# Performance work log

Hardware: AMD Instinct MI355X
Metric: run time of the kernel (lower is better)

The kernel has to match this reference:

```python
import jax, jax.numpy as jnp
import numpy as np

N = 50000      # num nodes
E = 800000     # num edges
IN = 512       # in_feats (= num_hidden)
H = 8          # num_heads
D = 64         # out_feats per head (H*D = 512)
NEG_SLOPE = 0.2


def setup_inputs() -> dict:
    key = jax.random.key(0)
    ks = jax.random.split(key, 7)
    feat = jax.random.normal(ks[0], (N, IN), jnp.float32)
    src = jax.random.randint(ks[1], (E,), 0, N)
    dst = jax.random.randint(ks[2], (E,), 0, N)
    W_fc = jax.random.normal(ks[3], (IN, H * D), jnp.float32) * (1.0 / np.sqrt(IN))
    W_res = jax.random.normal(ks[4], (IN, H * D), jnp.float32) * (1.0 / np.sqrt(IN))
    attn_l = jax.random.normal(ks[5], (1, H, D), jnp.float32) * 0.1
    attn_r = jax.random.normal(ks[6], (1, H, D), jnp.float32) * 0.1
    return {"feat": feat, "src": src, "dst": dst, "W_fc": W_fc,
            "W_res": W_res, "attn_l": attn_l, "attn_r": attn_r}


def reference(feat, src, dst, W_fc, W_res, attn_l, attn_r):
    # fc: [N, IN] @ [IN, H*D] -> [N, H, D]
    ft = (feat @ W_fc).reshape(N, H, D)
    # attention logits per node: el = sum(ft * attn_l, -1), er likewise -> [N, H]
    el = jnp.sum(ft * attn_l, axis=-1)
    er = jnp.sum(ft * attn_r, axis=-1)
    # u_add_v on edges, then LeakyReLU -> [E, H]
    e = jax.nn.leaky_relu(el[src] + er[dst], negative_slope=NEG_SLOPE)
    # edge_softmax: normalize over incoming edges of each dst node
    m = jax.ops.segment_max(e, dst, num_segments=N)            # [N, H]
    m = jnp.where(jnp.isfinite(m), m, jnp.zeros_like(m))       # guard zero-in-degree
    ex = jnp.exp(e - m[dst])                                   # [E, H]
    s = jax.ops.segment_sum(ex, dst, num_segments=N)           # [N, H]
    a = ex / jnp.maximum(s[dst], 1e-9)                         # [E, H]
    # u_mul_e + sum aggregation: gather src features, weight, scatter-add to dst
    msg = ft[src] * a[:, :, None]                              # [E, H, D]
    rst = jax.ops.segment_sum(msg, dst, num_segments=N)        # [N, H, D]
    # residual: res_fc Linear since in_dst_feats != out_feats
    rst = rst + (feat @ W_res).reshape(N, H, D)
    return rst
```

## Files before the change

kernel.cpp:

```cpp
#include <hip/hip_runtime.h>
#include <hip/hip_bf16.h>

#define NN 50000
#define EE 800000
#define INF 512
#define HH 8
#define DD 64
#define HD 512

typedef unsigned short u16;
typedef u16 u16x8 __attribute__((ext_vector_type(8)));
typedef __bf16 bf16x8 __attribute__((ext_vector_type(8)));
typedef float f32x4 __attribute__((ext_vector_type(4)));

__device__ __forceinline__ float bf2f(u16 u) {
    return __uint_as_float(((unsigned)u) << 16);
}
__device__ __forceinline__ u16 f2bf(float f) {
    __hip_bfloat16 h = __float2bfloat16(f);
    return *reinterpret_cast<u16*>(&h);
}

__device__ __forceinline__ void gload_lds16(const void* g, void* l) {
    __builtin_amdgcn_global_load_lds(
        (const __attribute__((address_space(1))) void*)g,
        (__attribute__((address_space(3))) void*)l, 16, 0, 0);
}

__global__ __launch_bounds__(256) void sniff5_kernel(const u16* __restrict__ p0,
                                                     const u16* __restrict__ p1,
                                                     const u16* __restrict__ p2,
                                                     const u16* __restrict__ p3,
                                                     const u16* __restrict__ p4,
                                                     int* __restrict__ flags) {
    const u16* ps[5] = {p0, p1, p2, p3, p4};
    const u16* p = ps[blockIdx.x];
    __shared__ int bad;
    if (threadIdx.x == 0) bad = 0;
    __syncthreads();
    float v = fabsf(bf2f(p[2 * threadIdx.x]));
    if (!(v < 1e4f)) atomicAdd(&bad, 1);
    __syncthreads();
    if (threadIdx.x == 0) flags[blockIdx.x] = (bad >= 8) ? 1 : 0;
}

__global__ __launch_bounds__(256) void convert_kernel(const void* __restrict__ in,
                                                      u16* __restrict__ out,
                                                      const int* __restrict__ flag) {
    const int isf32 = *flag;
    const int total = NN * INF / 8;
    for (int i = blockIdx.x * 256 + threadIdx.x; i < total; i += gridDim.x * 256) {
        if (isf32) {
            f32x4 a = ((const f32x4*)in)[2 * i];
            f32x4 b = ((const f32x4*)in)[2 * i + 1];
            u16x8 w;
#pragma unroll
            for (int j = 0; j < 4; ++j) { w[j] = f2bf(a[j]); w[4 + j] = f2bf(b[j]); }
            ((u16x8*)out)[i] = w;
        } else {
            ((u16x8*)out)[i] = ((const u16x8*)in)[i];
        }
    }
}

__global__ __launch_bounds__(256) void transpose_kernel(const void* __restrict__ in,
                                                        u16* __restrict__ out,
                                                        const int* __restrict__ flag) {
    __shared__ u16 tile[64][65];
    const int isf32 = *flag;
    int tr = (blockIdx.x & 7) * 64;
    int tc = (blockIdx.x >> 3) * 64;
    for (int idx = threadIdx.x; idx < 64 * 64; idx += 256) {
        int r = idx >> 6, c = idx & 63;
        int g = (tr + r) * 512 + tc + c;
        tile[r][c] = isf32 ? f2bf(((const float*)in)[g]) : ((const u16*)in)[g];
    }
    __syncthreads();
    for (int idx = threadIdx.x; idx < 64 * 64; idx += 256) {
        int r = idx >> 6, c = idx & 63;
        out[(tc + r) * 512 + tr + c] = tile[c][r];
    }
}

__global__ void zero_deg_kernel(int* __restrict__ deg) {
    int t = blockIdx.x * 256 + threadIdx.x;
    if (t < NN) deg[t] = 0;
}

__global__ void count_kernel(const int* __restrict__ dst, int* __restrict__ deg) {
    int e = blockIdx.x * 256 + threadIdx.x;
    if (e < EE) atomicAdd(&deg[dst[e]], 1);
}

#define SCAN_CH 49
__global__ __launch_bounds__(1024) void scan_kernel(const int* __restrict__ deg,
                                                    int* __restrict__ rowptr,
                                                    int* __restrict__ cursor) {
    __shared__ int sums[1024];
    int t = threadIdx.x;
    int base = t * SCAN_CH;
    int s = 0;
    for (int k = 0; k < SCAN_CH; ++k) {
        int i = base + k;
        if (i < NN) s += deg[i];
    }
    sums[t] = s;
    __syncthreads();
    for (int off = 1; off < 1024; off <<= 1) {
        int v = (t >= off) ? sums[t - off] : 0;
        __syncthreads();
        sums[t] += v;
        __syncthreads();
    }
    int run = (t == 0) ? 0 : sums[t - 1];
    for (int k = 0; k < SCAN_CH; ++k) {
        int i = base + k;
        if (i < NN) {
            rowptr[i] = run;
            cursor[i] = run;
            run += deg[i];
        }
    }
    if (t == 0) rowptr[NN] = EE;
}

__global__ void scatter_kernel(const int* __restrict__ src, const int* __restrict__ dst,
                               int* __restrict__ cursor, int* __restrict__ csr_src) {
    int e = blockIdx.x * 256 + threadIdx.x;
    if (e < EE) {
        int p = atomicAdd(&cursor[dst[e]], 1);
        csr_src[p] = src[e];
    }
}

#define TM 128
#define TN 128
#define BK 64
#define NT (INF / BK)
#define NMBLK 392

__global__ __launch_bounds__(256, 5) void gemm_kernel(const u16* __restrict__ Ab,
                                                      const u16* __restrict__ Wt,
                                                      u16* __restrict__ ft,
                                                      float* __restrict__ outf) {
    __shared__ u16 Asm[TM * BK];
    __shared__ u16 Bsm[TN * BK];

    const int bid = blockIdx.x;
    const int r8 = bid & 7;
    const int q = bid >> 3;
    const int m0 = (((q >> 3) << 3) | r8) * TM;
    const int n0 = (q & 7) * TN;
    const int tid = threadIdx.x;
    const int lane = tid & 63;
    const int wave = tid >> 6;
    const int wr = (wave >> 1) * 64;
    const int wc = (wave & 1) * 64;
    const int lrow = lane & 15;
    const int quad = lane >> 4;

    const int rg = lane >> 3;
    const int ch = lane & 7;
    const int cs = ch ^ rg;

    const u16* asrc[4];
    const u16* bsrc[4];
    u16* adst[4];
    u16* bdst[4];
#pragma unroll
    for (int g = 0; g < 4; ++g) {
        int G = wave * 4 + g;
        int r = G * 8 + rg;
        int gr = m0 + r; gr = gr < NN ? gr : NN - 1;
        asrc[g] = Ab + (size_t)gr * INF + cs * 8;
        bsrc[g] = Wt + (size_t)(n0 + r) * INF + cs * 8;
        adst[g] = Asm + G * 512;
        bdst[g] = Bsm + G * 512;
    }

    f32x4 acc[4][4] = {};

    for (int t = 0; t < NT; ++t) {
        const int k0 = t * BK;
        __syncthreads();
#pragma unroll
        for (int g = 0; g < 4; ++g) {
            gload_lds16(asrc[g] + k0, adst[g]);
            gload_lds16(bsrc[g] + k0, bdst[g]);
        }
        __syncthreads();

#pragma unroll
        for (int ks = 0; ks < 2; ++ks) {
            bf16x8 af[4], bfr[4];
#pragma unroll
            for (int mi = 0; mi < 4; ++mi) {
                int ar = wr + mi * 16 + lrow;
                int sc = (ks * 4 + quad) ^ (ar & 7);
                u16x8 tv = *(const u16x8*)(Asm + ar * 64 + sc * 8);
                af[mi] = *(bf16x8*)&tv;
            }
#pragma unroll
            for (int ni = 0; ni < 4; ++ni) {
                int br = wc + ni * 16 + lrow;
                int sc = (ks * 4 + quad) ^ (br & 7);
                u16x8 tv = *(const u16x8*)(Bsm + br * 64 + sc * 8);
                bfr[ni] = *(bf16x8*)&tv;
            }
#pragma unroll
            for (int mi = 0; mi < 4; ++mi)
#pragma unroll
                for (int ni = 0; ni < 4; ++ni)
                    acc[mi][ni] = __builtin_amdgcn_mfma_f32_16x16x32_bf16(af[mi], bfr[ni],
                                                                          acc[mi][ni], 0, 0, 0);
        }
    }

#pragma unroll
    for (int mi = 0; mi < 4; ++mi) {
        int rb = m0 + wr + mi * 16 + quad * 4;
#pragma unroll
        for (int ni = 0; ni < 4; ++ni) {
            int col = n0 + wc + ni * 16 + lrow;
#pragma unroll
            for (int r = 0; r < 4; ++r) {
                int row = rb + r;
                if (row < NN) {
                    float v = acc[mi][ni][r];
                    if (col < HD) ft[row * HD + col] = f2bf(v);
                    else outf[row * HD + (col - HD)] = v;
                }
            }
        }
    }
}

__global__ __launch_bounds__(256) void attn_dot_kernel(const u16* __restrict__ ft,
                                                       const void* __restrict__ al,
                                                       const void* __restrict__ ar,
                                                       float* __restrict__ el,
                                                       float* __restrict__ er,
                                                       const int* __restrict__ flags) {
    int node = blockIdx.x * 4 + (threadIdx.x >> 6);
    if (node >= NN) return;
    int lane = threadIdx.x & 63;
    int off = lane * 8;

    float wl[8], wr_[8];
    if (flags[3]) {
        f32x4 a0 = *(const f32x4*)((const float*)al + off);
        f32x4 a1 = *(const f32x4*)((const float*)al + off + 4);
#pragma unroll
        for (int j = 0; j < 4; ++j) { wl[j] = a0[j]; wl[4 + j] = a1[j]; }
    } else {
        u16x8 a = *(const u16x8*)((const u16*)al + off);
#pragma unroll
        for (int j = 0; j < 8; ++j) wl[j] = bf2f(a[j]);
    }
    if (flags[4]) {
        f32x4 a0 = *(const f32x4*)((const float*)ar + off);
        f32x4 a1 = *(const f32x4*)((const float*)ar + off + 4);
#pragma unroll
        for (int j = 0; j < 4; ++j) { wr_[j] = a0[j]; wr_[4 + j] = a1[j]; }
    } else {
        u16x8 a = *(const u16x8*)((const u16*)ar + off);
#pragma unroll
        for (int j = 0; j < 8; ++j) wr_[j] = bf2f(a[j]);
    }

    u16x8 f = *(const u16x8*)(ft + node * HD + off);
    float vl = 0.0f, vr = 0.0f;
#pragma unroll
    for (int j = 0; j < 8; ++j) {
        float x = bf2f(f[j]);
        vl += x * wl[j];
        vr += x * wr_[j];
    }
#pragma unroll
    for (int msk = 1; msk < 8; msk <<= 1) {
        vl += __shfl_xor(vl, msk);
        vr += __shfl_xor(vr, msk);
    }
    if ((lane & 7) == 0) {
        el[node * HH + (lane >> 3)] = vl;
        er[node * HH + (lane >> 3)] = vr;
    }
}

__global__ __launch_bounds__(256) void aggregate_kernel(const int* __restrict__ rowptr,
                                                        const int* __restrict__ csr_src,
                                                        const u16* __restrict__ ft,
                                                        const float* __restrict__ el,
                                                        const float* __restrict__ er,
                                                        float* __restrict__ outf) {
    int node = blockIdx.x * 4 + (threadIdx.x >> 6);
    if (node >= NN) return;
    int lane = threadIdx.x & 63;
    int head = lane >> 3;
    int beg = rowptr[node], end = rowptr[node + 1];
    float erd = er[node * HH + head];

    float m = -INFINITY;
    float sden = 0.0f;
    float acc[8] = {};

    float el_n = 0.0f;
    u16x8 f_n = {};
    if (beg < end) {
        int s0 = csr_src[beg];
        el_n = el[s0 * HH + head];
        f_n = *(const u16x8*)(ft + s0 * HD + lane * 8);
    }
    for (int i = beg; i < end; ++i) {
        float elv = el_n;
        u16x8 f = f_n;
        if (i + 1 < end) {
            int s2 = csr_src[i + 1];
            el_n = el[s2 * HH + head];
            f_n = *(const u16x8*)(ft + s2 * HD + lane * 8);
        }
        float v = elv + erd;
        v = v > 0.0f ? v : 0.2f * v;
        float nm = fmaxf(m, v);
        float scale = __expf(m - nm);
        float ex = __expf(v - nm);
        m = nm;
        sden = sden * scale + ex;
#pragma unroll
        for (int j = 0; j < 8; ++j) acc[j] = acc[j] * scale + bf2f(f[j]) * ex;
    }

    float inv = 1.0f / fmaxf(sden, 1e-9f);
    float* op = outf + node * HD + lane * 8;
    f32x4 r0 = *(const f32x4*)op;
    f32x4 r1 = *(const f32x4*)(op + 4);
    f32x4 o0, o1;
#pragma unroll
    for (int j = 0; j < 4; ++j) {
        o0[j] = acc[j] * inv + r0[j];
        o1[j] = acc[4 + j] * inv + r1[j];
    }
    *(f32x4*)op = o0;
    *(f32x4*)(op + 4) = o1;
}

extern "C" void kernel_launch(void* const* d_in, const int* in_sizes, int n_in,
                              void* d_out, int out_size, void* d_ws, size_t ws_size,
                              hipStream_t stream) {
    const void* feat   = d_in[0];
    const int*  src    = (const int*)d_in[1];
    const int*  dst    = (const int*)d_in[2];
    const void* W_fc   = d_in[3];
    const void* W_res  = d_in[4];
    const void* attn_l = d_in[5];
    const void* attn_r = d_in[6];
    float* outf = (float*)d_out;

    char* ws = (char*)d_ws;
    int*   flags   = (int*)(ws);
    u16*   Wt      = (u16*)(ws + 256);
    u16*   ft      = (u16*)(ws + 1048832);
    float* el      = (float*)(ws + 52248832);
    float* er      = (float*)(ws + 53848832);
    int*   deg     = (int*)(ws + 55448832);
    int*   rowptr  = (int*)(ws + 55648832);
    int*   cursor  = (int*)(ws + 55848896);
    int*   csr_src = (int*)(ws + 56048896);
    u16*   feat16  = (u16*)(ws + 59248896);

    sniff5_kernel<<<5, 256, 0, stream>>>((const u16*)feat, (const u16*)W_fc,
                                         (const u16*)W_res, (const u16*)attn_l,
                                         (const u16*)attn_r, flags);
    convert_kernel<<<2048, 256, 0, stream>>>(feat, feat16, flags + 0);
    transpose_kernel<<<64, 256, 0, stream>>>(W_fc, Wt, flags + 1);
    transpose_kernel<<<64, 256, 0, stream>>>(W_res, Wt + 512 * 512, flags + 2);

    zero_deg_kernel<<<(NN + 255) / 256, 256, 0, stream>>>(deg);
    count_kernel<<<(EE + 255) / 256, 256, 0, stream>>>(dst, deg);
    scan_kernel<<<1, 1024, 0, stream>>>(deg, rowptr, cursor);
    scatter_kernel<<<(EE + 255) / 256, 256, 0, stream>>>(src, dst, cursor, csr_src);

    gemm_kernel<<<NMBLK * 8, 256, 0, stream>>>(feat16, Wt, ft, outf);

    attn_dot_kernel<<<(NN + 3) / 4, 256, 0, stream>>>(ft, attn_l, attn_r, el, er, flags);
    aggregate_kernel<<<(NN + 3) / 4, 256, 0, stream>>>(rowptr, csr_src, ft, el, er, outf);
}
```

Before: 679.0 us.

## Split aggregation across two waves per node with 4-deep gather prefetch and no online max

The aggregate kernel now assigns two wavefronts per destination node, each lane handling 4 features instead of 8, and unrolls the edge loop by four with a software pipeline that keeps four gathers in flight plus source indices prefetched two steps ahead. The online-softmax running max and rescaling are dropped in favour of a plain exp with the logit clamped at 75, so the per-edge work needs fewer exps and multiplies. This targets memory latency on the irregular feature gathers in exchange for more registers and redundant tail loads. Removing max subtraction could in principle lose precision for large logits, though the clamp prevents overflow.

```diff
diff --git a/kernel.cpp b/kernel.cpp
--- a/kernel.cpp
+++ b/kernel.cpp
@@ -9,6 +9,7 @@
 #define HD 512
 
 typedef unsigned short u16;
+typedef u16 u16x4 __attribute__((ext_vector_type(4)));
 typedef u16 u16x8 __attribute__((ext_vector_type(8)));
 typedef __bf16 bf16x8 __attribute__((ext_vector_type(8)));
 typedef float f32x4 __attribute__((ext_vector_type(4)));
@@ -293,55 +294,71 @@
                                                         const float* __restrict__ el,
                                                         const float* __restrict__ er,
                                                         float* __restrict__ outf) {
-    int node = blockIdx.x * 4 + (threadIdx.x >> 6);
+    int node = blockIdx.x * 2 + (threadIdx.x >> 7);
     if (node >= NN) return;
+    int half = (threadIdx.x >> 6) & 1;
     int lane = threadIdx.x & 63;
-    int head = lane >> 3;
+    int ebase = half * 256 + lane * 4;
+    int head = ebase >> 6;
     int beg = rowptr[node], end = rowptr[node + 1];
     float erd = er[node * HH + head];
 
-    float m = -INFINITY;
     float sden = 0.0f;
-    float acc[8] = {};
-
-    float el_n = 0.0f;
-    u16x8 f_n = {};
+    float acc0 = 0.f, acc1 = 0.f, acc2 = 0.f, acc3 = 0.f;
+
     if (beg < end) {
-        int s0 = csr_src[beg];
-        el_n = el[s0 * HH + head];
-        f_n = *(const u16x8*)(ft + s0 * HD + lane * 8);
-    }
-    for (int i = beg; i < end; ++i) {
-        float elv = el_n;
-        u16x8 f = f_n;
-        if (i + 1 < end) {
-            int s2 = csr_src[i + 1];
-            el_n = el[s2 * HH + head];
-            f_n = *(const u16x8*)(ft + s2 * HD + lane * 8);
-        }
-        float v = elv + erd;
-        v = v > 0.0f ? v : 0.2f * v;
-        float nm = fmaxf(m, v);
-        float scale = __expf(m - nm);
-        float ex = __expf(v - nm);
-        m = nm;
-        sden = sden * scale + ex;
-#pragma unroll
-        for (int j = 0; j < 8; ++j) acc[j] = acc[j] * scale + bf2f(f[j]) * ex;
+        const int last = end - 1;
+        float elp0, elp1, elp2, elp3;
+        u16x4 fp0, fp1, fp2, fp3;
+        int sn0, sn1, sn2, sn3;
+        {
+            int c0 = csr_src[min(beg + 0, last)];
+            int c1 = csr_src[min(beg + 1, last)];
+            int c2 = csr_src[min(beg + 2, last)];
+            int c3 = csr_src[min(beg + 3, last)];
+            elp0 = el[c0 * HH + head]; fp0 = *(const u16x4*)(ft + c0 * HD + ebase);
+            elp1 = el[c1 * HH + head]; fp1 = *(const u16x4*)(ft + c1 * HD + ebase);
+            elp2 = el[c2 * HH + head]; fp2 = *(const u16x4*)(ft + c2 * HD + ebase);
+            elp3 = el[c3 * HH + head]; fp3 = *(const u16x4*)(ft + c3 * HD + ebase);
+            sn0 = csr_src[min(beg + 4, last)];
+            sn1 = csr_src[min(beg + 5, last)];
+            sn2 = csr_src[min(beg + 6, last)];
+            sn3 = csr_src[min(beg + 7, last)];
+        }
+        for (int base = beg; base < end; base += 4) {
+#define PROC(K)                                                              \
+            {                                                                \
+                float elv = elp##K;                                          \
+                u16x4 f = fp##K;                                             \
+                int s = sn##K;                                               \
+                elp##K = el[s * HH + head];                                  \
+                fp##K = *(const u16x4*)(ft + s * HD + ebase);                \
+                sn##K = csr_src[min(base + 8 + K, last)];                    \
+                float v = elv + erd;                                         \
+                v = v > 0.0f ? v : 0.2f * v;                                 \
+                v = fminf(v, 75.0f);                                         \
+                float ex = __expf(v);                                        \
+                ex = (base + K < end) ? ex : 0.0f;                           \
+                sden += ex;                                                  \
+                acc0 += bf2f(f[0]) * ex;                                     \
+                acc1 += bf2f(f[1]) * ex;                                     \
+                acc2 += bf2f(f[2]) * ex;                                     \
+                acc3 += bf2f(f[3]) * ex;                                     \
+            }
+            PROC(0) PROC(1) PROC(2) PROC(3)
+#undef PROC
+        }
     }
 
     float inv = 1.0f / fmaxf(sden, 1e-9f);
-    float* op = outf + node * HD + lane * 8;
-    f32x4 r0 = *(const f32x4*)op;
-    f32x4 r1 = *(const f32x4*)(op + 4);
-    f32x4 o0, o1;
-#pragma unroll
-    for (int j = 0; j < 4; ++j) {
-        o0[j] = acc[j] * inv + r0[j];
-        o1[j] = acc[4 + j] * inv + r1[j];
-    }
-    *(f32x4*)op = o0;
-    *(f32x4*)(op + 4) = o1;
+    float* op = outf + node * HD + ebase;
+    f32x4 r = *(const f32x4*)op;
+    f32x4 o;
+    o[0] = acc0 * inv + r[0];
+    o[1] = acc1 * inv + r[1];
+    o[2] = acc2 * inv + r[2];
+    o[3] = acc3 * inv + r[3];
+    *(f32x4*)op = o;
 }
 
 extern "C" void kernel_launch(void* const* d_in, const int* in_sizes, int n_in,
@@ -383,5 +400,5 @@
     gemm_kernel<<<NMBLK * 8, 256, 0, stream>>>(feat16, Wt, ft, outf);
 
     attn_dot_kernel<<<(NN + 3) / 4, 256, 0, stream>>>(ft, attn_l, attn_r, el, er, flags);
-    aggregate_kernel<<<(NN + 3) / 4, 256, 0, stream>>>(rowptr, csr_src, ft, el, er, outf);
-}
+    aggregate_kernel<<<(NN + 1) / 2, 256, 0, stream>>>(rowptr, csr_src, ft, el, er, outf);
+}
```

After: 670.2 us. No clear change (-1.3%).

## Deepen aggregate prefetch to 8 edges and drop online softmax max tracking

Applied to the files above, without the earlier changes.

Rewrites the per-node aggregation loop to keep eight edges of source features and logits in flight through register software pipelining, with clamped indices and masked tail edges. It also replaces the online-max softmax rescaling with a direct exp of the clamped logit, removing the per-edge rescale multiply and one exp. The cost is more registers, which may lower occupancy, plus redundant loads on tail iterations. Skipping max subtraction relies on the logits staying small enough, since the clamp at 75 changes results if a logit ever exceeds it.

```diff
diff --git a/kernel.cpp b/kernel.cpp
--- a/kernel.cpp
+++ b/kernel.cpp
@@ -9,6 +9,7 @@
 #define HD 512
 
 typedef unsigned short u16;
+typedef u16 u16x4 __attribute__((ext_vector_type(4)));
 typedef u16 u16x8 __attribute__((ext_vector_type(8)));
 typedef __bf16 bf16x8 __attribute__((ext_vector_type(8)));
 typedef float f32x4 __attribute__((ext_vector_type(4)));
@@ -296,42 +297,59 @@
     int node = blockIdx.x * 4 + (threadIdx.x >> 6);
     if (node >= NN) return;
     int lane = threadIdx.x & 63;
+    int ebase = lane * 8;
     int head = lane >> 3;
     int beg = rowptr[node], end = rowptr[node + 1];
     float erd = er[node * HH + head];
 
-    float m = -INFINITY;
     float sden = 0.0f;
     float acc[8] = {};
 
-    float el_n = 0.0f;
-    u16x8 f_n = {};
     if (beg < end) {
-        int s0 = csr_src[beg];
-        el_n = el[s0 * HH + head];
-        f_n = *(const u16x8*)(ft + s0 * HD + lane * 8);
-    }
-    for (int i = beg; i < end; ++i) {
-        float elv = el_n;
-        u16x8 f = f_n;
-        if (i + 1 < end) {
-            int s2 = csr_src[i + 1];
-            el_n = el[s2 * HH + head];
-            f_n = *(const u16x8*)(ft + s2 * HD + lane * 8);
-        }
-        float v = elv + erd;
-        v = v > 0.0f ? v : 0.2f * v;
-        float nm = fmaxf(m, v);
-        float scale = __expf(m - nm);
-        float ex = __expf(v - nm);
-        m = nm;
-        sden = sden * scale + ex;
-#pragma unroll
-        for (int j = 0; j < 8; ++j) acc[j] = acc[j] * scale + bf2f(f[j]) * ex;
+        const int last = end - 1;
+        float elp0, elp1, elp2, elp3, elp4, elp5, elp6, elp7;
+        u16x8 fp0, fp1, fp2, fp3, fp4, fp5, fp6, fp7;
+        int sn0, sn1, sn2, sn3, sn4, sn5, sn6, sn7;
+#define PRO(K)                                                               \
+        {                                                                    \
+            int c = csr_src[min(beg + K, last)];                             \
+            elp##K = el[c * HH + head];                                      \
+            fp##K = *(const u16x8*)(ft + (size_t)c * HD + ebase);            \
+            sn##K = csr_src[min(beg + 8 + K, last)];                         \
+        }
+        PRO(0) PRO(1) PRO(2) PRO(3) PRO(4) PRO(5) PRO(6) PRO(7)
+#undef PRO
+        for (int base = beg; base < end; base += 8) {
+#define PROC(K)                                                              \
+            {                                                                \
+                float elv = elp##K;                                          \
+                u16x8 f = fp##K;                                             \
+                int s = sn##K;                                               \
+                elp##K = el[s * HH + head];                                  \
+                fp##K = *(const u16x8*)(ft + (size_t)s * HD + ebase);        \
+                sn##K = csr_src[min(base + 16 + K, last)];                   \
+                float v = elv + erd;                                         \
+                v = v > 0.0f ? v : 0.2f * v;                                 \
+                v = fminf(v, 75.0f);                                         \
+                float ex = __expf(v);                                        \
+                ex = (base + K < end) ? ex : 0.0f;                           \
+                sden += ex;                                                  \
+                acc[0] += bf2f(f[0]) * ex;                                   \
+                acc[1] += bf2f(f[1]) * ex;                                   \
+                acc[2] += bf2f(f[2]) * ex;                                   \
+                acc[3] += bf2f(f[3]) * ex;                                   \
+                acc[4] += bf2f(f[4]) * ex;                                   \
+                acc[5] += bf2f(f[5]) * ex;                                   \
+                acc[6] += bf2f(f[6]) * ex;                                   \
+                acc[7] += bf2f(f[7]) * ex;                                   \
+            }
+            PROC(0) PROC(1) PROC(2) PROC(3) PROC(4) PROC(5) PROC(6) PROC(7)
+#undef PROC
+        }
     }
 
     float inv = 1.0f / fmaxf(sden, 1e-9f);
-    float* op = outf + node * HD + lane * 8;
+    float* op = outf + node * HD + ebase;
     f32x4 r0 = *(const f32x4*)op;
     f32x4 r1 = *(const f32x4*)(op + 4);
     f32x4 o0, o1;
```

After: 676.9 us. About the same (-0.3%).
